# Optimization experiments

Measured on AMD Instinct MI355X. Metric: run time of the kernel, lower is better.

## Reference

```python
import jax, jax.numpy as jnp
import numpy as np

DIM = 2048
N_HEADS = 16
N_KV_HEADS = 8
HEAD_DIM = DIM // N_HEADS  # 128
N_REP = N_HEADS // N_KV_HEADS
BATCH = 2
SEQ = 2048
CHUNK = 128  # chunked-parallel causal linear attention; SEQ % CHUNK == 0


def _make_freqs_cis(seq_len, head_dim, theta=10000.0):
    freqs = 1.0 / (theta ** (np.arange(0, head_dim, 2, dtype=np.float32) / head_dim))
    t = np.arange(seq_len, dtype=np.float32)
    ang = np.outer(t, freqs)  # [S, D/2]
    return jnp.asarray(np.stack([np.cos(ang), np.sin(ang)], axis=-1))  # [S, D/2, 2]


def setup_inputs() -> dict:
    key = jax.random.key(0)
    ks = jax.random.split(key, 5)
    x = jax.random.normal(ks[0], (BATCH, SEQ, DIM), dtype=jnp.float32)
    freqs_cis = _make_freqs_cis(SEQ, HEAD_DIM)
    s = 0.02
    wq = s * jax.random.normal(ks[1], (N_HEADS * HEAD_DIM, DIM), dtype=jnp.float32)
    wk = s * jax.random.normal(ks[2], (N_KV_HEADS * HEAD_DIM, DIM), dtype=jnp.float32)
    wv = s * jax.random.normal(ks[3], (N_KV_HEADS * HEAD_DIM, DIM), dtype=jnp.float32)
    wo = s * jax.random.normal(ks[4], (DIM, N_HEADS * HEAD_DIM), dtype=jnp.float32)
    return {"x": x, "freqs_cis": freqs_cis, "wq": wq, "wk": wk, "wv": wv, "wo": wo}


def _apply_rotary(x, freqs_cis):
    # x: [B, S, H, D]; freqs_cis: [S, D/2, 2] (cos, sin). Llama pairing: (x0,x1),(x2,x3),...
    B, S, H, D = x.shape
    xr = x.reshape(B, S, H, D // 2, 2)
    x0, x1 = xr[..., 0], xr[..., 1]
    c = freqs_cis[None, :, None, :, 0]
    s = freqs_cis[None, :, None, :, 1]
    o0 = x0 * c - x1 * s
    o1 = x0 * s + x1 * c
    return jnp.stack([o0, o1], axis=-1).reshape(B, S, H, D)


def _causal_linear_attention(q, k, v):
    # q, k, v: [B, H, S, D]; output_i = q_i @ sum_{j<=i} k_j^T v_j
    B, H, S, D = q.shape
    q = jax.nn.softmax(q * (D ** -0.5), axis=-1)  # softmax over feature dim
    k = jax.nn.softmax(k, axis=2)                 # softmax over sequence dim (as in source)
    Nc = S // CHUNK
    qc = q.reshape(B, H, Nc, CHUNK, D)
    kc = k.reshape(B, H, Nc, CHUNK, D)
    vc = v.reshape(B, H, Nc, CHUNK, D)
    # per-chunk KV outer-product sums: [B, H, Nc, D, D]
    kv = jnp.einsum('bhncd,bhnce->bhnde', kc, vc)
    cum = jnp.cumsum(kv, axis=2)
    cum_excl = jnp.concatenate([jnp.zeros_like(cum[:, :, :1]), cum[:, :, :-1]], axis=2)
    inter = jnp.einsum('bhncd,bhnde->bhnce', qc, cum_excl)
    scores = jnp.einsum('bhncd,bhnmd->bhncm', qc, kc)  # [B,H,Nc,C,C]
    mask = jnp.tril(jnp.ones((CHUNK, CHUNK), dtype=bool))
    scores = jnp.where(mask, scores, jnp.zeros((), dtype=scores.dtype))
    intra = jnp.einsum('bhncm,bhnme->bhnce', scores, vc)
    return (inter + intra).reshape(B, H, S, D)


def reference(x, freqs_cis, wq, wk, wv, wo):
    B, S, _ = x.shape
    xq = (x @ wq.T).reshape(B, S, N_HEADS, HEAD_DIM)
    xk = (x @ wk.T).reshape(B, S, N_KV_HEADS, HEAD_DIM)
    xv = (x @ wv.T).reshape(B, S, N_KV_HEADS, HEAD_DIM)
    xq = _apply_rotary(xq, freqs_cis)
    xk = _apply_rotary(xk, freqs_cis)
    # repeat_kv: each kv head repeated N_REP consecutive times
    keys = jnp.repeat(xk, N_REP, axis=2)
    values = jnp.repeat(xv, N_REP, axis=2)
    q = jnp.transpose(xq, (0, 2, 1, 3))
    k = jnp.transpose(keys, (0, 2, 1, 3))
    v = jnp.transpose(values, (0, 2, 1, 3))
    out = _causal_linear_attention(q, k, v)  # [B, H, S, D]
    out = jnp.transpose(out, (0, 2, 1, 3)).reshape(B, S, N_HEADS * HEAD_DIM)
    return out @ wo.T
```

## Files before the change

### kernel.cpp

```cpp
#include <hip/hip_runtime.h>
#include <math.h>

#define DIMV 2048
#define NHEAD 16
#define NKV 8
#define HD 128
#define BATCH 2
#define SEQ 2048
#define CHUNK 128
#define NCHUNK 16
#define MTOK 4096
#define KVD (NKV * HD)

typedef _Float16 half8_t __attribute__((ext_vector_type(8)));
typedef _Float16 half4_t __attribute__((ext_vector_type(4)));
typedef _Float16 half2_t __attribute__((ext_vector_type(2)));
typedef float f32x4 __attribute__((ext_vector_type(4)));

#define GLOBAL_AS __attribute__((address_space(1)))
#define LDS_AS __attribute__((address_space(3)))

#define BARX() __builtin_amdgcn_s_barrier()
#define WAITL(n) asm volatile("s_waitcnt lgkmcnt(" #n ")" ::: "memory")
#define WAITVM(n) asm volatile("s_waitcnt vmcnt(" #n ")" ::: "memory")

__global__ __launch_bounds__(256) void cast_all(const float* __restrict__ x,
                                                const float* __restrict__ wq,
                                                const float* __restrict__ wk,
                                                const float* __restrict__ wv,
                                                const float* __restrict__ wo,
                                                _Float16* __restrict__ xh,
                                                _Float16* __restrict__ wqkvh,
                                                _Float16* __restrict__ woh) {
  long i = (long)(blockIdx.x * 256 + threadIdx.x) * 8;
  const float* src;
  _Float16* dst;
  long off;
  if (i < 8388608)        { src = x;  dst = xh;              off = 0; }
  else if (i < 12582912)  { src = wq; dst = wqkvh;           off = 8388608; }
  else if (i < 14680064)  { src = wk; dst = wqkvh + 4194304; off = 12582912; }
  else if (i < 16777216)  { src = wv; dst = wqkvh + 6291456; off = 14680064; }
  else                    { src = wo; dst = woh;             off = 16777216; }
  long e = i - off;
  float4 a = *(const float4*)&src[e];
  float4 b = *(const float4*)&src[e + 4];
  half8_t h = {(_Float16)a.x, (_Float16)a.y, (_Float16)a.z, (_Float16)a.w,
               (_Float16)b.x, (_Float16)b.y, (_Float16)b.z, (_Float16)b.w};
  *(half8_t*)&dst[e] = h;
}

__global__ __launch_bounds__(256) void transpose_fc(const float* __restrict__ fc,
                                                    float* __restrict__ fcT) {
  __shared__ float T[64][65];
  int s0 = blockIdx.x * 64, d0 = blockIdx.y * 64;
  int t = threadIdx.x;
  int r = t >> 4, c4 = (t & 15) * 4;
#pragma unroll
  for (int p = 0; p < 4; ++p) {
    int sr = p * 16 + r;
    float4 v = *(const float4*)&fc[(size_t)(s0 + sr) * 128 + d0 + c4];
    T[sr][c4] = v.x; T[sr][c4 + 1] = v.y; T[sr][c4 + 2] = v.z; T[sr][c4 + 3] = v.w;
  }
  __syncthreads();
#pragma unroll
  for (int p = 0; p < 4; ++p) {
    int dr = p * 16 + r;
    float4 v = make_float4(T[c4][dr], T[c4 + 1][dr], T[c4 + 2][dr], T[c4 + 3][dr]);
    *(float4*)&fcT[(size_t)(d0 + dr) * SEQ + s0 + c4] = v;
  }
}

#define STG_A(bb, kk, i, k0)                                                      \
  __builtin_amdgcn_global_load_lds(                                               \
      (const GLOBAL_AS void*)(A + aoff + (size_t)(i) * 128 * 2048 + (k0) + (kk) * 32), \
      (LDS_AS void*)(As + ((bb) * 2 + (kk)) * 8192 + (i) * 4096 + wave * 512), 16, 0, 0)
#define STG_B(bb, kk, i, k0)                                                      \
  __builtin_amdgcn_global_load_lds(                                               \
      (const GLOBAL_AS void*)(B + boff + (size_t)(i) * 128 * 2048 + (k0) + (kk) * 32), \
      (LDS_AS void*)(Bs + ((bb) * 2 + (kk)) * 8192 + (i) * 4096 + wave * 512), 16, 0, 0)

#define LDA_F(bb, kk, ih) do {                                                    \
    const _Float16* pA_ = As + ((bb) * 2 + (kk)) * 8192 +                         \
                          (wr * 128 + (ih) * 64 + m16) * 32 + pseg8;              \
    af[0] = *(const half8_t*)(pA_);                                               \
    af[1] = *(const half8_t*)(pA_ + 512);                                         \
    af[2] = *(const half8_t*)(pA_ + 1024);                                        \
    af[3] = *(const half8_t*)(pA_ + 1536);                                        \
  } while (0)
#define LDB_F(bb, kk) do {                                                        \
    const _Float16* pB_ = Bs + ((bb) * 2 + (kk)) * 8192 +                         \
                          (wc * 64 + m16) * 32 + pseg8;                           \
    bf[0] = *(const half8_t*)(pB_);                                               \
    bf[1] = *(const half8_t*)(pB_ + 512);                                         \
    bf[2] = *(const half8_t*)(pB_ + 1024);                                        \
    bf[3] = *(const half8_t*)(pB_ + 1536);                                        \
  } while (0)

#define MMX(ih) do {                                                              \
    _Pragma("unroll")                                                             \
    for (int i_ = 0; i_ < 4; ++i_)                                                \
      _Pragma("unroll")                                                           \
      for (int j_ = 0; j_ < 4; ++j_)                                              \
        acc[(ih) * 4 + i_][j_] = __builtin_amdgcn_mfma_f32_16x16x32_f16(          \
            af[i_], bf[j_], acc[(ih) * 4 + i_][j_], 0, 0, 0);                     \
  } while (0)

#define KTILE(bb, k0, DS1, DS2, DS3, DS4, VA, VB) do {                            \
  half8_t af[4], bf[4];                                                           \
                                                           \
  LDA_F(bb, 0, 0); LDB_F(bb, 0);                                                  \
  if (DS1) { STG_A(1 - (bb), 1, 0, (k0) + 64); STG_A(1 - (bb), 1, 1, (k0) + 64); } \
  BARX(); WAITL(0);                                                               \
  __builtin_amdgcn_s_setprio(1); MMX(0); __builtin_amdgcn_s_setprio(0);           \
  BARX();                                                                         \
                                                \
  LDA_F(bb, 0, 1);                                                                \
  if (DS2) { STG_B(1 - (bb), 1, 0, (k0) + 64); STG_B(1 - (bb), 1, 1, (k0) + 64); } \
  WAITVM(VA);                                                                     \
  BARX(); WAITL(0);                                                               \
  __builtin_amdgcn_s_setprio(1); MMX(1); __builtin_amdgcn_s_setprio(0);           \
  BARX();                                                                         \
                                                           \
  LDA_F(bb, 1, 0); LDB_F(bb, 1);                                                  \
  if (DS3) { STG_A(bb, 0, 0, (k0) + 128); STG_A(bb, 0, 1, (k0) + 128); }          \
  BARX(); WAITL(0);                                                               \
  __builtin_amdgcn_s_setprio(1); MMX(0); __builtin_amdgcn_s_setprio(0);           \
  BARX();                                                                         \
                                                \
  LDA_F(bb, 1, 1);                                                                \
  if (DS4) { STG_B(bb, 0, 0, (k0) + 128); STG_B(bb, 0, 1, (k0) + 128); }          \
  WAITVM(VB);                                                                     \
  BARX(); WAITL(0);                                                               \
  __builtin_amdgcn_s_setprio(1); MMX(1); __builtin_amdgcn_s_setprio(0);           \
  BARX();                                                                         \
} while (0)

__global__ __launch_bounds__(512, 2) void hgemm_qkv_8p(const _Float16* __restrict__ A,
                                                       const _Float16* __restrict__ B,
                                                       const float* __restrict__ fc,
                                                       _Float16* __restrict__ qh,
                                                       _Float16* __restrict__ kT,
                                                       _Float16* __restrict__ vT) {
  const int K = 2048;
  __shared__ _Float16 As[32768];
  __shared__ _Float16 Bs[32768];
  __shared__ float qsum[4][256];

  const int tid = threadIdx.x;
  const int lane = tid & 63;
  const int wave = tid >> 6;
  const int wr = wave >> 2;
  const int wc = wave & 3;
  const int m16 = lane & 15, quad = lane >> 4;
  const int row0 = blockIdx.y * 256, col0 = blockIdx.x * 256;
  const int pseg8 = (quad ^ ((m16 >> 1) & 3)) * 8;

  const int r_ld = tid >> 2;
  const int sseg = (tid & 3) ^ ((tid >> 3) & 3);
  const size_t aoff = (size_t)(row0 + r_ld) * K + sseg * 8;
  const size_t boff = (size_t)(col0 + r_ld) * K + sseg * 8;

  f32x4 acc[8][4];
#pragma unroll
  for (int m = 0; m < 8; ++m)
#pragma unroll
    for (int j = 0; j < 4; ++j) acc[m][j] = (f32x4){0.f, 0.f, 0.f, 0.f};

  STG_A(0, 0, 0, 0); STG_A(0, 0, 1, 0); STG_B(0, 0, 0, 0); STG_B(0, 0, 1, 0);
  STG_A(0, 1, 0, 0); STG_A(0, 1, 1, 0); STG_B(0, 1, 0, 0); STG_B(0, 1, 1, 0);
  STG_A(1, 0, 0, 64); STG_A(1, 0, 1, 64); STG_B(1, 0, 0, 64); STG_B(1, 0, 1, 64);
  WAITVM(8);
  BARX();

  for (int t = 0; t < 30; t += 2) {
    KTILE(0, t * 64,      1, 1, 1, 1, 8, 8);
    KTILE(1, t * 64 + 64, 1, 1, 1, 1, 8, 8);
  }
  KTILE(0, 1920, 1, 1, 0, 0, 8, 4);
  KTILE(1, 1984, 0, 0, 0, 0, 0, 0);

  if (col0 < 2048) {
    const float sc = 0.08838834764831845f;
    float psum[8][4];
#pragma unroll
    for (int m = 0; m < 8; ++m)
#pragma unroll
      for (int r = 0; r < 4; ++r) psum[m][r] = 0.f;
#pragma unroll
    for (int m = 0; m < 8; ++m)
#pragma unroll
      for (int j = 0; j < 4; ++j) {
        int dl2 = (wc * 64 + j * 16 + m16) & 126;
#pragma unroll
        for (int r = 0; r < 4; ++r) {
          float val = acc[m][j][r];
          float par = __shfl_xor(val, 1);
          int row_l = wr * 128 + (m >> 2) * 64 + (m & 3) * 16 + quad * 4 + r;
          int s_tok = (row0 + row_l) & (SEQ - 1);
          float2 cs = *(const float2*)&fc[(size_t)s_tok * 128 + dl2];
          float o = val * cs.x + par * ((m16 & 1) ? cs.y : -cs.y);
          float e = __expf(o * sc);
          acc[m][j][r] = e;
          psum[m][r] += e;
        }
      }
#pragma unroll
    for (int mm = 1; mm < 16; mm <<= 1)
#pragma unroll
      for (int m = 0; m < 8; ++m)
#pragma unroll
        for (int r = 0; r < 4; ++r) psum[m][r] += __shfl_xor(psum[m][r], mm);
    if (m16 == 0) {
#pragma unroll
      for (int m = 0; m < 8; ++m)
#pragma unroll
        for (int r = 0; r < 4; ++r) {
          int row_l = wr * 128 + (m >> 2) * 64 + (m & 3) * 16 + quad * 4 + r;
          qsum[wc][row_l] = psum[m][r];
        }
    }
    __syncthreads();
#pragma unroll
    for (int m = 0; m < 8; ++m)
#pragma unroll
      for (int r = 0; r < 4; ++r) {
        int row_l = wr * 128 + (m >> 2) * 64 + (m & 3) * 16 + quad * 4 + r;
        psum[m][r] = 1.f / (qsum[wc & 2][row_l] + qsum[(wc & 2) | 1][row_l]);
      }
#pragma unroll
    for (int m = 0; m < 8; ++m)
#pragma unroll
      for (int j = 0; j < 4; ++j) {
        int col = col0 + wc * 64 + j * 16 + m16;
#pragma unroll
        for (int r = 0; r < 4; ++r) {
          int row_l = wr * 128 + (m >> 2) * 64 + (m & 3) * 16 + quad * 4 + r;
          qh[(size_t)(row0 + row_l) * DIMV + col] = (_Float16)(acc[m][j][r] * psum[m][r]);
        }
      }
  } else {
#pragma unroll
    for (int m = 0; m < 8; ++m)
#pragma unroll
      for (int j = 0; j < 4; ++j) {
        int col = col0 + wc * 64 + j * 16 + m16;
        int rowb = row0 + wr * 128 + (m >> 2) * 64 + (m & 3) * 16 + quad * 4;
        half4_t hv = {(_Float16)acc[m][j][0], (_Float16)acc[m][j][1],
                      (_Float16)acc[m][j][2], (_Float16)acc[m][j][3]};
        if (col0 < 3072) {
          *(half4_t*)&kT[(size_t)(col - 2048) * MTOK + rowb] = hv;
        } else {
          *(half4_t*)&vT[(size_t)(col - 3072) * MTOK + rowb] = hv;
        }
      }
  }
}

__global__ __launch_bounds__(256) void hgemm_bt64_f32(const _Float16* __restrict__ A,
                                                      const _Float16* __restrict__ B,
                                                      float* __restrict__ C,
                                                      int M, int N, int K) {
  __shared__ _Float16 As[128 * 64];
  __shared__ _Float16 Bs[128 * 64];
  const int tid = threadIdx.x;
  const int lane = tid & 63;
  const int wave = tid >> 6;
  const int row0 = blockIdx.y * 128, col0 = blockIdx.x * 128;
  const int wr = wave & 1, wc = wave >> 1;
  const int m16 = lane & 15, quad = lane >> 4;

  f32x4 acc[4][4];
#pragma unroll
  for (int i = 0; i < 4; ++i)
#pragma unroll
    for (int j = 0; j < 4; ++j) acc[i][j] = (f32x4){0.f, 0.f, 0.f, 0.f};

  const int r_ld = tid >> 3;
  const int sseg = (tid & 7) ^ (r_ld & 7);
  const size_t a_base = (size_t)(row0 + r_ld) * K + sseg * 8;
  const size_t b_base = (size_t)(col0 + r_ld) * K + sseg * 8;
  _Float16* ldsA = As + wave * 512;
  _Float16* ldsB = Bs + wave * 512;
  const int swzA = quad ^ (m16 & 7);

  for (int k0 = 0; k0 < K; k0 += 64) {
#pragma unroll
    for (int i = 0; i < 4; ++i) {
      __builtin_amdgcn_global_load_lds(
          (const GLOBAL_AS void*)(A + a_base + (size_t)i * 32 * K + k0),
          (LDS_AS void*)(ldsA + i * 2048), 16, 0, 0);
      __builtin_amdgcn_global_load_lds(
          (const GLOBAL_AS void*)(B + b_base + (size_t)i * 32 * K + k0),
          (LDS_AS void*)(ldsB + i * 2048), 16, 0, 0);
    }
    __syncthreads();
#pragma unroll
    for (int kk = 0; kk < 2; ++kk) {
      const int swz = swzA ^ (kk * 4);
      half8_t af[4], bf[4];
#pragma unroll
      for (int i = 0; i < 4; ++i) {
        af[i] = *(half8_t*)&As[(wr * 64 + i * 16 + m16) * 64 + swz * 8];
        bf[i] = *(half8_t*)&Bs[(wc * 64 + i * 16 + m16) * 64 + swz * 8];
      }
#pragma unroll
      for (int i = 0; i < 4; ++i)
#pragma unroll
        for (int j = 0; j < 4; ++j)
          acc[i][j] = __builtin_amdgcn_mfma_f32_16x16x32_f16(af[i], bf[j], acc[i][j], 0, 0, 0);
    }
    __syncthreads();
  }

#pragma unroll
  for (int i = 0; i < 4; ++i)
#pragma unroll
    for (int j = 0; j < 4; ++j) {
      int col = col0 + wc * 64 + j * 16 + m16;
      int rowb = row0 + wr * 64 + i * 16 + quad * 4;
#pragma unroll
      for (int r = 0; r < 4; ++r) C[(size_t)(rowb + r) * N + col] = acc[i][j][r];
    }
}

__global__ __launch_bounds__(256) void k_rope_softmax_T(_Float16* __restrict__ kT,
                                                        const float* __restrict__ fcT) {
  int bi = blockIdx.x;
  int b = bi & 1, pr = bi >> 1;
  int d0 = pr * 2, dl = d0 & 127;
  int t = threadIdx.x;
  size_t r0 = (size_t)d0 * MTOK + b * SEQ + t * 8;
  size_t r1 = r0 + MTOK;
  half8_t x0v = *(half8_t*)&kT[r0];
  half8_t x1v = *(half8_t*)&kT[r1];
  int s8 = t * 8;
  float4 ca = *(const float4*)&fcT[(size_t)dl * SEQ + s8];
  float4 cb = *(const float4*)&fcT[(size_t)dl * SEQ + s8 + 4];
  float4 sa = *(const float4*)&fcT[(size_t)(dl + 1) * SEQ + s8];
  float4 sb = *(const float4*)&fcT[(size_t)(dl + 1) * SEQ + s8 + 4];
  float cc[8] = {ca.x, ca.y, ca.z, ca.w, cb.x, cb.y, cb.z, cb.w};
  float ss[8] = {sa.x, sa.y, sa.z, sa.w, sb.x, sb.y, sb.z, sb.w};
  float e0[8], e1[8];
  float sum0 = 0.f, sum1 = 0.f;
#pragma unroll
  for (int j = 0; j < 8; ++j) {
    float x0 = (float)x0v[j], x1 = (float)x1v[j];
    float o0 = x0 * cc[j] - x1 * ss[j];
    float o1 = x0 * ss[j] + x1 * cc[j];
    e0[j] = expf(o0); e1[j] = expf(o1);
    sum0 += e0[j]; sum1 += e1[j];
  }
#pragma unroll
  for (int off = 1; off < 64; off <<= 1) {
    sum0 += __shfl_xor(sum0, off);
    sum1 += __shfl_xor(sum1, off);
  }
  __shared__ float red[8];
  if ((t & 63) == 0) { red[(t >> 6) * 2] = sum0; red[(t >> 6) * 2 + 1] = sum1; }
  __syncthreads();
  float S0 = red[0] + red[2] + red[4] + red[6];
  float S1 = red[1] + red[3] + red[5] + red[7];
  float i0 = 1.f / S0, i1 = 1.f / S1;
  half8_t w0, w1;
#pragma unroll
  for (int j = 0; j < 8; ++j) {
    w0[j] = (_Float16)(e0[j] * i0);
    w1[j] = (_Float16)(e1[j] * i1);
  }
  *(half8_t*)&kT[r0] = w0;
  *(half8_t*)&kT[r1] = w1;
}

__global__ __launch_bounds__(256) void transpose_k(const _Float16* __restrict__ kT,
                                                   _Float16* __restrict__ kh) {
  __shared__ _Float16 T[64][65];
  int t0 = blockIdx.x * 64, d0 = blockIdx.y * 64;
  int t = threadIdx.x;
  int r = t >> 3, c8 = (t & 7) * 8;
#pragma unroll
  for (int p = 0; p < 2; ++p) {
    int dr = p * 32 + r;
    half8_t v = *(const half8_t*)&kT[(size_t)(d0 + dr) * MTOK + t0 + c8];
#pragma unroll
    for (int j = 0; j < 8; ++j) T[c8 + j][dr] = v[j];
  }
  __syncthreads();
#pragma unroll
  for (int p = 0; p < 2; ++p) {
    int tr = p * 32 + r;
    half8_t v;
#pragma unroll
    for (int j = 0; j < 8; ++j) v[j] = T[tr][c8 + j];
    *(half8_t*)&kh[(size_t)(t0 + tr) * KVD + d0 + c8] = v;
  }
}

__global__ __launch_bounds__(256) void kv_chunk_mfma(const _Float16* __restrict__ vT,
                                                     const _Float16* __restrict__ kT,
                                                     float* __restrict__ kvT) {
  __shared__ _Float16 As[2][128 * 32];
  __shared__ _Float16 Bs[2][128 * 32];
  int bi = blockIdx.x;
  int n = bi & 15, kvh = (bi >> 4) & 7, b = bi >> 7;
  int tok0 = b * SEQ + n * CHUNK;
  const int tid = threadIdx.x;
  const int lane = tid & 63;
  const int wave = tid >> 6;
  const int wr = wave & 1, wc = wave >> 1;
  const int m16 = lane & 15, quad = lane >> 4;
  const int qsw8 = (quad ^ ((m16 >> 1) & 3)) * 8;

  f32x4 acc[4][4];
#pragma unroll
  for (int i = 0; i < 4; ++i)
#pragma unroll
    for (int j = 0; j < 4; ++j) acc[i][j] = (f32x4){0.f, 0.f, 0.f, 0.f};

  const int r_ld = tid >> 2;
  const int sseg = (tid & 3) ^ ((tid >> 3) & 3);
  const size_t a_base = (size_t)(kvh * HD + r_ld) * MTOK + tok0 + sseg * 8;

#pragma unroll
  for (int i = 0; i < 2; ++i) {
    __builtin_amdgcn_global_load_lds(
        (const GLOBAL_AS void*)(vT + a_base + (size_t)i * 64 * MTOK),
        (LDS_AS void*)(&As[0][0] + i * 2048 + wave * 512), 16, 0, 0);
    __builtin_amdgcn_global_load_lds(
        (const GLOBAL_AS void*)(kT + a_base + (size_t)i * 64 * MTOK),
        (LDS_AS void*)(&Bs[0][0] + i * 2048 + wave * 512), 16, 0, 0);
  }

#pragma unroll
  for (int s = 0; s < 4; ++s) {
    WAITVM(0);
    BARX();
    if (s < 3) {
      const int k0 = (s + 1) * 32;
      const int bb = (s + 1) & 1;
#pragma unroll
      for (int i = 0; i < 2; ++i) {
        __builtin_amdgcn_global_load_lds(
            (const GLOBAL_AS void*)(vT + a_base + (size_t)i * 64 * MTOK + k0),
            (LDS_AS void*)(&As[bb][0] + i * 2048 + wave * 512), 16, 0, 0);
        __builtin_amdgcn_global_load_lds(
            (const GLOBAL_AS void*)(kT + a_base + (size_t)i * 64 * MTOK + k0),
            (LDS_AS void*)(&Bs[bb][0] + i * 2048 + wave * 512), 16, 0, 0);
      }
    }
    const _Float16* ra = &As[s & 1][0];
    const _Float16* rb = &Bs[s & 1][0];
    half8_t af[4], bf[4];
#pragma unroll
    for (int i = 0; i < 4; ++i) {
      af[i] = *(const half8_t*)&ra[(wr * 64 + i * 16 + m16) * 32 + qsw8];
      bf[i] = *(const half8_t*)&rb[(wc * 64 + i * 16 + m16) * 32 + qsw8];
    }
#pragma unroll
    for (int i = 0; i < 4; ++i)
#pragma unroll
      for (int j = 0; j < 4; ++j)
        acc[i][j] = __builtin_amdgcn_mfma_f32_16x16x32_f16(af[i], bf[j], acc[i][j], 0, 0, 0);
  }
#pragma unroll
  for (int i = 0; i < 4; ++i)
#pragma unroll
    for (int j = 0; j < 4; ++j) {
      int col = wc * 64 + j * 16 + m16;
      int rowb = wr * 64 + i * 16 + quad * 4;
#pragma unroll
      for (int r = 0; r < 4; ++r)
        kvT[(size_t)bi * 16384 + (size_t)(rowb + r) * 128 + col] = acc[i][j][r];
    }
}

__global__ __launch_bounds__(256) void cumsum_h(const float* __restrict__ kvT,
                                                _Float16* __restrict__ cumh) {
  int gid = blockIdx.x * 256 + threadIdx.x;
  int bk = gid >> 14, idx = gid & 16383;
  size_t base = (size_t)bk * NCHUNK * 16384 + idx;
  float run = 0.f;
#pragma unroll
  for (int n = 0; n < NCHUNK; ++n) {
    cumh[base + (size_t)n * 16384] = (_Float16)run;
    run += kvT[base + (size_t)n * 16384];
  }
}

__global__ __launch_bounds__(256) void attn_fused(const _Float16* __restrict__ qh,
                                                  const _Float16* __restrict__ kh,
                                                  const _Float16* __restrict__ cumh,
                                                  const _Float16* __restrict__ vT,
                                                  _Float16* __restrict__ ath) {
  __shared__ _Float16 Qs[128 * 128];
  __shared__ _Float16 Bs[2][128 * 32];
  __shared__ _Float16 Ss[128 * 128];
  int bi = blockIdx.x;
  int n = bi & 15, h = (bi >> 4) & 15, b = bi >> 8;
  int kvh = h >> 1;
  int tok0 = b * SEQ + n * CHUNK;
  const int tid = threadIdx.x;
  const int lane = tid & 63;
  const int wave = tid >> 6;
  const int wr = wave & 1, wc = wave >> 1;
  const int m16 = lane & 15, quad = lane >> 4;
  const int qsw8 = (quad ^ ((m16 >> 1) & 3)) * 8;
  const int r_ld = tid >> 2;
  const int sseg = (tid & 3) ^ ((tid >> 3) & 3);

  f32x4 acc[4][4];
#pragma unroll
  for (int i = 0; i < 4; ++i)
#pragma unroll
    for (int j = 0; j < 4; ++j) acc[i][j] = (f32x4){0.f, 0.f, 0.f, 0.f};

  const int qrow = tid >> 4;
  const int qsl = (tid & 15) ^ (qrow & 7);
  const size_t qsrc = (size_t)(tok0 + qrow) * DIMV + h * HD + qsl * 8;
#pragma unroll
  for (int p = 0; p < 8; ++p)
    __builtin_amdgcn_global_load_lds(
        (const GLOBAL_AS void*)(qh + qsrc + (size_t)p * 16 * DIMV),
        (LDS_AS void*)(Qs + p * 2048 + wave * 512), 16, 0, 0);

  const size_t kbase = (size_t)(tok0 + r_ld) * KVD + kvh * HD + sseg * 8;
  const size_t cbase = ((size_t)((b * 8 + kvh) * 16 + n)) * 16384 + (size_t)r_ld * 128 + sseg * 8;
  const size_t vbase = (size_t)(kvh * HD + r_ld) * MTOK + tok0 + sseg * 8;

#pragma unroll
  for (int i = 0; i < 2; ++i)
    __builtin_amdgcn_global_load_lds(
        (const GLOBAL_AS void*)(kh + kbase + (size_t)i * 64 * KVD),
        (LDS_AS void*)(&Bs[0][0] + i * 2048 + wave * 512), 16, 0, 0);

#pragma unroll
  for (int s = 0; s < 12; ++s) {
    WAITVM(0);
    BARX();
    if (s < 11) {
      const int sn = s + 1;
      _Float16* dstB = &Bs[sn & 1][0];
      if (sn < 4) {
        const int k0 = sn * 32;
#pragma unroll
        for (int i = 0; i < 2; ++i)
          __builtin_amdgcn_global_load_lds(
              (const GLOBAL_AS void*)(kh + kbase + (size_t)i * 64 * KVD + k0),
              (LDS_AS void*)(dstB + i * 2048 + wave * 512), 16, 0, 0);
      } else if (sn < 8) {
        const int k0 = (sn - 4) * 32;
#pragma unroll
        for (int i = 0; i < 2; ++i)
          __builtin_amdgcn_global_load_lds(
              (const GLOBAL_AS void*)(cumh + cbase + (size_t)i * 64 * 128 + k0),
              (LDS_AS void*)(dstB + i * 2048 + wave * 512), 16, 0, 0);
      } else {
        const int k0 = (sn - 8) * 32;
#pragma unroll
        for (int i = 0; i < 2; ++i)
          __builtin_amdgcn_global_load_lds(
              (const GLOBAL_AS void*)(vT + vbase + (size_t)i * 64 * MTOK + k0),
              (LDS_AS void*)(dstB + i * 2048 + wave * 512), 16, 0, 0);
      }
    }
    half8_t af[4], bf[4];
    const _Float16* rb = &Bs[s & 1][0];
#pragma unroll
    for (int i = 0; i < 4; ++i)
      bf[i] = *(const half8_t*)&rb[(wc * 64 + i * 16 + m16) * 32 + qsw8];
    if (s < 8) {
      const int sl4 = (s & 3) * 4;
#pragma unroll
      for (int i = 0; i < 4; ++i) {
        int row = wr * 64 + i * 16 + m16;
        af[i] = *(const half8_t*)&Qs[row * 128 + ((sl4 + quad) ^ (m16 & 7)) * 8];
      }
    } else {
      const int sl4 = (s - 8) * 4;
#pragma unroll
      for (int i = 0; i < 4; ++i) {
        int row = wr * 64 + i * 16 + m16;
        af[i] = *(const half8_t*)&Ss[row * 128 + ((sl4 + quad) ^ (m16 & 7)) * 8];
      }
    }
#pragma unroll
    for (int i = 0; i < 4; ++i)
#pragma unroll
      for (int j = 0; j < 4; ++j)
        acc[i][j] = __builtin_amdgcn_mfma_f32_16x16x32_f16(af[i], bf[j], acc[i][j], 0, 0, 0);
    if (s == 3) {
#pragma unroll
      for (int i = 0; i < 4; ++i)
#pragma unroll
        for (int j = 0; j < 4; ++j) {
          int col = wc * 64 + j * 16 + m16;
          int rowb = wr * 64 + i * 16 + quad * 4;
#pragma unroll
          for (int r = 0; r < 4; ++r) {
            int row = rowb + r;
            float v = (col <= row) ? acc[i][j][r] : 0.f;
            int sp = (col >> 3) ^ (row & 7);
            Ss[row * 128 + sp * 8 + (col & 7)] = (_Float16)v;
          }
          acc[i][j] = (f32x4){0.f, 0.f, 0.f, 0.f};
        }
      WAITL(0);
    }
  }

#pragma unroll
  for (int i = 0; i < 4; ++i)
#pragma unroll
    for (int j = 0; j < 4; ++j) {
      int col = wc * 64 + j * 16 + m16;
      int rowb = wr * 64 + i * 16 + quad * 4;
#pragma unroll
      for (int r = 0; r < 4; ++r)
        ath[(size_t)(tok0 + rowb + r) * DIMV + h * HD + col] = (_Float16)acc[i][j][r];
    }
}

extern "C" void kernel_launch(void* const* d_in, const int* in_sizes, int n_in,
                              void* d_out, int out_size, void* d_ws, size_t ws_size,
                              hipStream_t stream) {
  const float* x  = (const float*)d_in[0];
  const float* fc = (const float*)d_in[1];
  const float* wq = (const float*)d_in[2];
  const float* wk = (const float*)d_in[3];
  const float* wv = (const float*)d_in[4];
  const float* wo = (const float*)d_in[5];
  float* out = (float*)d_out;

  char* p = (char*)d_ws;
  _Float16* xh    = (_Float16*)p;  p += 16777216;
  _Float16* wqkvh = (_Float16*)p;  p += 16777216;
  _Float16* woh   = (_Float16*)p;  p += 8388608;
  _Float16* qh    = (_Float16*)p;  p += 16777216;
  _Float16* kT    = (_Float16*)p;  p += 8388608;
  _Float16* kh    = (_Float16*)p;  p += 8388608;
  _Float16* vT    = (_Float16*)p;  p += 8388608;
  float*    kvT   = (float*)p;     p += 16777216;
  _Float16* cumh  = (_Float16*)p;  p += 8388608;
  _Float16* ath   = (_Float16*)p;  p += 16777216;
  float*    fcT   = (float*)p;     p += 1048576;

  cast_all<<<10240, 256, 0, stream>>>(x, wq, wk, wv, wo, xh, wqkvh, woh);
  transpose_fc<<<dim3(32, 2), 256, 0, stream>>>(fc, fcT);

  hgemm_qkv_8p<<<dim3(16, 16), 512, 0, stream>>>(xh, wqkvh, fc, qh, kT, vT);

  k_rope_softmax_T<<<1024, 256, 0, stream>>>(kT, fcT);
  transpose_k<<<dim3(64, 16), 256, 0, stream>>>(kT, kh);

  kv_chunk_mfma<<<256, 256, 0, stream>>>(vT, kT, kvT);
  cumsum_h<<<1024, 256, 0, stream>>>(kvT, cumh);
  attn_fused<<<512, 256, 0, stream>>>(qh, kh, cumh, vT, ath);

  hgemm_bt64_f32<<<dim3(16, 32), 256, 0, stream>>>(ath, woh, out, MTOK, 2048, 2048);
}
```

Measured before the change: 294.9 us.

## Replace output projection GEMM with 8-wave multi-stage pipelined kernel

Rewrites the final output-projection GEMM as a 512-thread kernel with a 128x256 tile and a four-slot LDS ring of half-K (32) stages. Global-to-LDS loads for future stages are issued inside each compute phase and gated with vmcnt waits, so memory latency overlaps MFMA work. It also raises MFMA issue priority around the compute block. The larger tile halves the block count (256 blocks) and uses more LDS, which may reduce occupancy and leave some CUs idle.

```diff
diff --git a/kernel.cpp b/kernel.cpp
--- a/kernel.cpp
+++ b/kernel.cpp
@@ -256,18 +256,62 @@
   }
 }
 
-__global__ __launch_bounds__(256) void hgemm_bt64_f32(const _Float16* __restrict__ A,
+#define STGBT(bb, kk, k0) do {                                                    \
+  __builtin_amdgcn_global_load_lds(                                               \
+      (const GLOBAL_AS void*)(A + abase + (k0) + (kk) * 32),                      \
+      (LDS_AS void*)(As + ((bb) * 2 + (kk)) * 4096 + wave * 512), 16, 0, 0);      \
+  __builtin_amdgcn_global_load_lds(                                               \
+      (const GLOBAL_AS void*)(B + bbase + (k0) + (kk) * 32),                      \
+      (LDS_AS void*)(Bs + ((bb) * 2 + (kk)) * 8192 + wave * 512), 16, 0, 0);      \
+  __builtin_amdgcn_global_load_lds(                                               \
+      (const GLOBAL_AS void*)(B + bbase + (size_t)128 * 2048 + (k0) + (kk) * 32), \
+      (LDS_AS void*)(Bs + ((bb) * 2 + (kk)) * 8192 + 4096 + wave * 512), 16, 0, 0);\
+} while (0)
+
+#define PHASE_BT(bb, kk, SEN, sbb, skk, sk0, VM) do {                             \
+  WAITVM(VM);                                                                     \
+  BARX();                                                                         \
+  half8_t af[4], bf[4];                                                           \
+  const _Float16* pA_ = As + ((bb) * 2 + (kk)) * 4096 +                           \
+                        (wr * 64 + m16) * 32 + pseg8;                             \
+  const _Float16* pB_ = Bs + ((bb) * 2 + (kk)) * 8192 +                           \
+                        (wc * 64 + m16) * 32 + pseg8;                             \
+  af[0] = *(const half8_t*)(pA_);        af[1] = *(const half8_t*)(pA_ + 512);    \
+  af[2] = *(const half8_t*)(pA_ + 1024); af[3] = *(const half8_t*)(pA_ + 1536);   \
+  bf[0] = *(const half8_t*)(pB_);        bf[1] = *(const half8_t*)(pB_ + 512);    \
+  bf[2] = *(const half8_t*)(pB_ + 1024); bf[3] = *(const half8_t*)(pB_ + 1536);   \
+  if (SEN) STGBT(sbb, skk, sk0);                                                  \
+  WAITL(0);                                                                       \
+  __builtin_amdgcn_s_setprio(1);                                                  \
+  _Pragma("unroll")                                                               \
+  for (int i_ = 0; i_ < 4; ++i_)                                                  \
+    _Pragma("unroll")                                                             \
+    for (int j_ = 0; j_ < 4; ++j_)                                                \
+      acc[i_][j_] = __builtin_amdgcn_mfma_f32_16x16x32_f16(                       \
+          af[i_], bf[j_], acc[i_][j_], 0, 0, 0);                                  \
+  __builtin_amdgcn_s_setprio(0);                                                  \
+} while (0)
+
+__global__ __launch_bounds__(512, 2) void hgemm_bt_8p(const _Float16* __restrict__ A,
                                                       const _Float16* __restrict__ B,
-                                                      float* __restrict__ C,
-                                                      int M, int N, int K) {
-  __shared__ _Float16 As[128 * 64];
-  __shared__ _Float16 Bs[128 * 64];
+                                                      float* __restrict__ C) {
+  const int K = 2048, N = 2048;
+  __shared__ _Float16 As[16384];
+  __shared__ _Float16 Bs[32768];
+
   const int tid = threadIdx.x;
   const int lane = tid & 63;
   const int wave = tid >> 6;
-  const int row0 = blockIdx.y * 128, col0 = blockIdx.x * 128;
-  const int wr = wave & 1, wc = wave >> 1;
+  const int wr = wave >> 2;
+  const int wc = wave & 3;
   const int m16 = lane & 15, quad = lane >> 4;
+  const int row0 = blockIdx.y * 128, col0 = blockIdx.x * 256;
+  const int pseg8 = (quad ^ ((m16 >> 1) & 3)) * 8;
+
+  const int r_ld = tid >> 2;
+  const int sseg = (tid & 3) ^ ((tid >> 3) & 3);
+  const size_t abase = (size_t)(row0 + r_ld) * K + sseg * 8;
+  const size_t bbase = (size_t)(col0 + r_ld) * K + sseg * 8;
 
   f32x4 acc[4][4];
 #pragma unroll
@@ -275,42 +319,18 @@
 #pragma unroll
     for (int j = 0; j < 4; ++j) acc[i][j] = (f32x4){0.f, 0.f, 0.f, 0.f};
 
-  const int r_ld = tid >> 3;
-  const int sseg = (tid & 7) ^ (r_ld & 7);
-  const size_t a_base = (size_t)(row0 + r_ld) * K + sseg * 8;
-  const size_t b_base = (size_t)(col0 + r_ld) * K + sseg * 8;
-  _Float16* ldsA = As + wave * 512;
-  _Float16* ldsB = Bs + wave * 512;
-  const int swzA = quad ^ (m16 & 7);
-
-  for (int k0 = 0; k0 < K; k0 += 64) {
-#pragma unroll
-    for (int i = 0; i < 4; ++i) {
-      __builtin_amdgcn_global_load_lds(
-          (const GLOBAL_AS void*)(A + a_base + (size_t)i * 32 * K + k0),
-          (LDS_AS void*)(ldsA + i * 2048), 16, 0, 0);
-      __builtin_amdgcn_global_load_lds(
-          (const GLOBAL_AS void*)(B + b_base + (size_t)i * 32 * K + k0),
-          (LDS_AS void*)(ldsB + i * 2048), 16, 0, 0);
-    }
-    __syncthreads();
-#pragma unroll
-    for (int kk = 0; kk < 2; ++kk) {
-      const int swz = swzA ^ (kk * 4);
-      half8_t af[4], bf[4];
-#pragma unroll
-      for (int i = 0; i < 4; ++i) {
-        af[i] = *(half8_t*)&As[(wr * 64 + i * 16 + m16) * 64 + swz * 8];
-        bf[i] = *(half8_t*)&Bs[(wc * 64 + i * 16 + m16) * 64 + swz * 8];
-      }
-#pragma unroll
-      for (int i = 0; i < 4; ++i)
-#pragma unroll
-        for (int j = 0; j < 4; ++j)
-          acc[i][j] = __builtin_amdgcn_mfma_f32_16x16x32_f16(af[i], bf[j], acc[i][j], 0, 0, 0);
-    }
-    __syncthreads();
-  }
+  STGBT(0, 0, 0); STGBT(0, 1, 0); STGBT(1, 0, 64);
+
+  for (int t = 0; t < 30; ++t) {
+    const int bb = t & 1;
+    const int k0 = t * 64;
+    PHASE_BT(bb, 0, 1, bb ^ 1, 1, k0 + 64, 6);
+    PHASE_BT(bb, 1, 1, bb, 0, k0 + 128, 6);
+  }
+  PHASE_BT(0, 0, 1, 1, 1, 1984, 6);
+  PHASE_BT(0, 1, 0, 0, 0, 0, 6);
+  PHASE_BT(1, 0, 0, 0, 0, 0, 3);
+  PHASE_BT(1, 1, 0, 0, 0, 0, 0);
 
 #pragma unroll
   for (int i = 0; i < 4; ++i)
@@ -655,5 +675,5 @@
   cumsum_h<<<1024, 256, 0, stream>>>(kvT, cumh);
   attn_fused<<<512, 256, 0, stream>>>(qh, kh, cumh, vT, ath);
 
-  hgemm_bt64_f32<<<dim3(16, 32), 256, 0, stream>>>(ath, woh, out, MTOK, 2048, 2048);
-}
+  hgemm_bt_8p<<<dim3(8, 32), 512, 0, stream>>>(ath, woh, out);
+}
```

After: 287.2 us. 2.6% less time.
